# Kernel optimization log

Measured on AMD Instinct MI355X. Metric: run time of the kernel, lower is better.

## Reference

```python
import jax, jax.numpy as jnp
import numpy as np

HEADS = 16
LN_EPS = 1e-6

def _layernorm(x, scale, bias):
    mu = jnp.mean(x, axis=-1, keepdims=True)
    var = jnp.mean(jnp.square(x - mu), axis=-1, keepdims=True)
    return (x - mu) * jax.lax.rsqrt(var + LN_EPS) * scale + bias

def setup_inputs() -> dict:
    key = jax.random.key(0)
    ks = jax.random.split(key, 5)
    B, L, D, F = 2, 2048, 1024, 4096
    s = lambda fan_in: 1.0 / np.sqrt(fan_in)
    return {
        'x': jax.random.normal(ks[0], (B, L, D), jnp.float32),
        'ln1_scale': jnp.ones((D,), jnp.float32),
        'ln1_bias': jnp.zeros((D,), jnp.float32),
        'w_qkv': jax.random.normal(ks[1], (D, 3 * D), jnp.float32) * s(D),
        'w_proj': jax.random.normal(ks[2], (D, D), jnp.float32) * s(D),
        'b_proj': jnp.zeros((D,), jnp.float32),
        'ln2_scale': jnp.ones((D,), jnp.float32),
        'ln2_bias': jnp.zeros((D,), jnp.float32),
        'w_mlp1': jax.random.normal(ks[3], (D, F), jnp.float32) * s(D),
        'b_mlp1': jnp.zeros((F,), jnp.float32),
        'w_mlp2': jax.random.normal(ks[4], (F, D), jnp.float32) * s(F),
        'b_mlp2': jnp.zeros((D,), jnp.float32),
    }

def reference(x, ln1_scale, ln1_bias, w_qkv, w_proj, b_proj,
              ln2_scale, ln2_bias, w_mlp1, b_mlp1, w_mlp2, b_mlp2):
    B, L, D = x.shape
    H = HEADS
    hd = D // H
    # pre-norm attention
    h = _layernorm(x, ln1_scale, ln1_bias)
    qkv = h @ w_qkv  # [B,L,3D]
    q, k, v = jnp.split(qkv, 3, axis=-1)
    q = q.reshape(B, L, H, hd).transpose(0, 2, 1, 3)  # [B,H,L,hd]
    k = k.reshape(B, L, H, hd).transpose(0, 2, 1, 3)
    v = v.reshape(B, L, H, hd).transpose(0, 2, 1, 3)
    scale = jnp.sqrt(jnp.float32(hd))
    scores = jnp.einsum('bhqd,bhkd->bhqk', q, k) / scale  # [B,H,L,L]
    attn = jax.nn.softmax(scores, axis=-1)
    out = jnp.einsum('bhqk,bhkd->bhqd', attn, v)  # [B,H,L,hd]
    out = out.transpose(0, 2, 1, 3).reshape(B, L, D)
    x = x + out @ w_proj + b_proj
    # pre-norm MLP
    h = _layernorm(x, ln2_scale, ln2_bias)
    m = jax.nn.gelu(h @ w_mlp1 + b_mlp1, approximate=True)
    return x + m @ w_mlp2 + b_mlp2
```

## Files before the change

### kernel.cpp

```cpp
#include <hip/hip_runtime.h>
#include <hip/hip_bf16.h>
#include <cstdint>
#include <cstddef>

typedef __bf16 bf16;
typedef __bf16 bf16x8 __attribute__((ext_vector_type(8)));
typedef float f32x4 __attribute__((ext_vector_type(4)));
typedef short short4v __attribute__((ext_vector_type(4)));
typedef unsigned uint2v __attribute__((ext_vector_type(2)));
typedef unsigned uint4v __attribute__((ext_vector_type(4)));

#define GLB_AS(p) ((const __attribute__((address_space(1))) unsigned*)(unsigned long long)(p))
#define LDS_AS(p) ((__attribute__((address_space(3))) unsigned*)(unsigned)(unsigned long long)(p))

__device__ __forceinline__ void g2l16(const void* g, void* l) {
  __builtin_amdgcn_global_load_lds(GLB_AS(g), LDS_AS(l), 16, 0, 0);
}

__device__ __forceinline__ short f2bf(float x) {
  bf16 h = (bf16)x;
  return __builtin_bit_cast(short, h);
}

__device__ __forceinline__ unsigned pk_bf16(float a, float b) {
  __hip_bfloat162 h = __float22bfloat162_rn(float2{a, b});
  unsigned u;
  __builtin_memcpy(&u, &h, 4);
  return u;
}

extern "C" __device__ __attribute__((const)) float __ocml_native_exp2_f32(float);
extern "C" __device__ __attribute__((const)) float __ocml_native_recip_f32(float);
__device__ __forceinline__ float fast_exp2(float x) {
  return __ocml_native_exp2_f32(x);
}
__device__ __forceinline__ float fast_tanh(float a) {
  float e = __ocml_native_exp2_f32(a * 2.8853900817779268f);
  return 1.f - 2.f * __ocml_native_recip_f32(e + 1.f);
}

constexpr int MROWS = 4096;
constexpr size_t ATILE = (size_t)MROWS * 32;

#define QSCALE 0.18033688011112042f

__device__ __forceinline__ void transpose_body(
    const float* __restrict__ in, bf16* __restrict__ out, int K, int N,
    int bx, int by, float (*tile)[33], int tid)
{
  int tx = tid & 31, ty = tid >> 5;
  int n0 = bx * 32, k0 = by * 32;
  for (int i = ty; i < 32; i += 8)
    tile[i][tx] = in[(size_t)(k0 + i) * N + n0 + tx];
  __syncthreads();
  bf16* obase = out + (size_t)(k0 >> 5) * N * 32;
  for (int i = ty; i < 32; i += 8)
    obase[(size_t)(n0 + i) * 32 + tx] = (bf16)tile[tx][i];
}

__device__ __forceinline__ void ln_body(
    const float* __restrict__ x, const float* __restrict__ sc,
    const float* __restrict__ bi, bf16* __restrict__ out,
    int row, float* wsum, float* wsq, int tid)
{
  const float* xr = x + (size_t)row * 1024;
  int c = tid * 4;
  float4 xv = *(const float4*)(xr + c);
  float s = xv.x + xv.y + xv.z + xv.w;
  float q = xv.x * xv.x + xv.y * xv.y + xv.z * xv.z + xv.w * xv.w;
#pragma unroll
  for (int off = 1; off < 64; off <<= 1) {
    s += __shfl_xor(s, off);
    q += __shfl_xor(q, off);
  }
  int wv = tid >> 6;
  if ((tid & 63) == 0) { wsum[wv] = s; wsq[wv] = q; }
  __syncthreads();
  s = wsum[0] + wsum[1] + wsum[2] + wsum[3];
  q = wsq[0] + wsq[1] + wsq[2] + wsq[3];
  float mean = s * (1.f / 1024.f);
  float var = q * (1.f / 1024.f) - mean * mean;
  float rstd = rsqrtf(var + 1e-6f);
  float4 scv = *(const float4*)(sc + c);
  float4 biv = *(const float4*)(bi + c);
  bf16* o = out + (size_t)(c >> 5) * ATILE + (size_t)row * 32 + (c & 31);
  o[0] = (bf16)((xv.x - mean) * rstd * scv.x + biv.x);
  o[1] = (bf16)((xv.y - mean) * rstd * scv.y + biv.y);
  o[2] = (bf16)((xv.z - mean) * rstd * scv.z + biv.z);
  o[3] = (bf16)((xv.w - mean) * rstd * scv.w + biv.w);
}

__global__ __launch_bounds__(256) void prep_kernel(
    const float* __restrict__ wqkv, const float* __restrict__ wproj,
    const float* __restrict__ wmlp1, const float* __restrict__ wmlp2,
    bf16* __restrict__ wqkv_t, bf16* __restrict__ wproj_t,
    bf16* __restrict__ wmlp1_t, bf16* __restrict__ wmlp2_t,
    const float* __restrict__ x, const float* __restrict__ ln1s,
    const float* __restrict__ ln1b, bf16* __restrict__ hbuf)
{
  __shared__ float tile[32][33];
  __shared__ float wsum[4], wsq[4];
  int bid = blockIdx.x, tid = threadIdx.x;
  if (bid < 3072)
    transpose_body(wqkv, wqkv_t, 1024, 3072, bid % 96, bid / 96, tile, tid);
  else if (bid < 4096) {
    int i = bid - 3072;
    transpose_body(wproj, wproj_t, 1024, 1024, i % 32, i / 32, tile, tid);
  } else if (bid < 8192) {
    int i = bid - 4096;
    transpose_body(wmlp1, wmlp1_t, 1024, 4096, i % 128, i / 128, tile, tid);
  } else if (bid < 12288) {
    int i = bid - 8192;
    transpose_body(wmlp2, wmlp2_t, 4096, 1024, i % 32, i / 32, tile, tid);
  } else {
    ln_body(x, ln1s, ln1b, hbuf, bid - 12288, wsum, wsq, tid);
  }
}

__global__ __launch_bounds__(256) void ln_kernel(
    const float* __restrict__ x, const float* __restrict__ sc,
    const float* __restrict__ bi, bf16* __restrict__ out)
{
  __shared__ float wsum[4], wsq[4];
  ln_body(x, sc, bi, out, blockIdx.x, wsum, wsq, threadIdx.x);
}

template <int MT, int NT, int KS, int EPI>
__global__ __launch_bounds__(256) void gemm_tt(
    const bf16* __restrict__ A, const bf16* __restrict__ Bt,
    int N, int K,
    const float* __restrict__ bias, const float* __restrict__ resid,
    float* __restrict__ outf, bf16* __restrict__ ob0,
    bf16* __restrict__ ob1, bf16* __restrict__ ob2)
{
  constexpr int TM = MT * 32, TN = NT * 32;
  __shared__ __align__(16) bf16 As[2][TM * 32 * KS];
  __shared__ __align__(16) bf16 Bs[2][TN * 32 * KS];
  const int tid = threadIdx.x, lane = tid & 63, wave = tid >> 6;
  const int wm = wave >> 1, wn = wave & 1;
  const int quad = lane >> 4, l16 = lane & 15;

  int flat = blockIdx.x + gridDim.x * blockIdx.y;
  int xcd = flat & 7, rr = flat >> 3;
  int npx = gridDim.x >> 3;
  int bn = xcd * npx + (rr % npx);
  int bm = rr / npx;

  const size_t astride = ATILE;
  const size_t bstride = (size_t)N * 32;
  const bf16* Abase = A + (size_t)bm * TM * 32 + (size_t)lane * 8;
  const bf16* Bbase = Bt + (size_t)bn * TN * 32 + (size_t)lane * 8;

  f32x4 acc[MT][NT] = {};
  const int KT = K / (32 * KS);

  auto stage = [&](int buf, int kt) {
#pragma unroll
    for (int ks = 0; ks < KS; ks++) {
      const bf16* Ab = Abase + (size_t)(kt * KS + ks) * astride;
      const bf16* Bb = Bbase + (size_t)(kt * KS + ks) * bstride;
#pragma unroll
      for (int i = 0; i < MT / 2; i++)
        g2l16(Ab + (wave + 4 * i) * 512, &As[buf][ks * TM * 32 + (wave + 4 * i) * 512]);
#pragma unroll
      for (int i = 0; i < NT / 2; i++)
        g2l16(Bb + (wave + 4 * i) * 512, &Bs[buf][ks * TN * 32 + (wave + 4 * i) * 512]);
    }
  };

  stage(0, 0);
  int buf = 0;
  for (int kt = 0; kt < KT; kt++) {
    __syncthreads();
    if (kt + 1 < KT) stage(buf ^ 1, kt + 1);
#pragma unroll
    for (int kk = 0; kk < KS; kk++) {
      bf16x8 af[MT], bfr[NT];
#pragma unroll
      for (int mt = 0; mt < MT; mt++)
        af[mt] = *(const bf16x8*)&As[buf][kk * TM * 32 + (wm * MT * 16 + mt * 16 + l16) * 32 + quad * 8];
#pragma unroll
      for (int nt = 0; nt < NT; nt++)
        bfr[nt] = *(const bf16x8*)&Bs[buf][kk * TN * 32 + (wn * NT * 16 + nt * 16 + l16) * 32 + quad * 8];
#pragma unroll
      for (int mt = 0; mt < MT; mt++)
#pragma unroll
        for (int nt = 0; nt < NT; nt++)
          acc[mt][nt] = __builtin_amdgcn_mfma_f32_16x16x32_bf16(af[mt], bfr[nt], acc[mt][nt], 0, 0, 0);
    }
    buf ^= 1;
  }

#pragma unroll
  for (int mt = 0; mt < MT; mt++) {
#pragma unroll
    for (int nt = 0; nt < NT; nt++) {
      int row0 = bm * TM + wm * MT * 16 + mt * 16 + quad * 4;
      int col = bn * TN + wn * NT * 16 + nt * 16 + l16;
      if (EPI == 0) {
        int b = row0 >> 11, l = row0 & 2047;
        int which = col >> 10, d = col & 1023;
        int hh = d >> 6, hdi = d & 63;
        size_t bh = (size_t)(b * 16 + hh);
        if (which == 0) {
#pragma unroll
          for (int r = 0; r < 4; r++)
            ob0[(bh * 2048 + l + r) * 64 + hdi] = (bf16)(acc[mt][nt][r] * QSCALE);
        } else if (which == 1) {
#pragma unroll
          for (int r = 0; r < 4; r++)
            ob1[(bh * 2048 + l + r) * 64 + hdi] = (bf16)acc[mt][nt][r];
        } else {
          short4v v4;
#pragma unroll
          for (int r = 0; r < 4; r++) v4[r] = f2bf(acc[mt][nt][r]);
          *(short4v*)&ob2[(bh * 64 + hdi) * 2048 + l] = v4;
        }
      } else {
#pragma unroll
        for (int r = 0; r < 4; r++) {
          int row = row0 + r;
          float v = acc[mt][nt][r];
          if (EPI == 1) {
            size_t idx = (size_t)row * N + col;
            outf[idx] = v + bias[col] + resid[idx];
          } else {
            float t = v + bias[col];
            float a = 0.7978845608028654f * t * (1.f + 0.044715f * t * t);
            float g = 0.5f * t * (1.f + fast_tanh(a));
            ob0[(size_t)(col >> 5) * ATILE + (size_t)row * 32 + (col & 31)] = (bf16)g;
          }
        }
      }
    }
  }
}

__global__ __launch_bounds__(512, 2) void gemm8p_gelu(
    const bf16* __restrict__ A, const bf16* __restrict__ Bt,
    const float* __restrict__ bias, bf16* __restrict__ ob0)
{
  __shared__ __align__(16) bf16 As[4 * 8192];
  __shared__ __align__(16) bf16 Bs[4 * 8192];
  const int tid = threadIdx.x, lane = tid & 63, wave = tid >> 6;
  const int quad = lane >> 4, l16 = lane & 15;
  const int wm = wave >> 2, wn = wave & 3;

  int flat = blockIdx.x + gridDim.x * blockIdx.y;
  int xcd = flat & 7, rr = flat >> 3;
  int bn = xcd * 2 + (rr & 1);
  int bm = rr >> 1;

  auto stA = [&](int buf, int ktile, int half) {
    const bf16* g = A + (size_t)ktile * ATILE +
                    ((size_t)bm * 256 + half * 128) * 32 + (size_t)tid * 8;
    g2l16(g, &As[(buf * 2 + (ktile & 1)) * 8192 + half * 4096 + wave * 512]);
  };
  auto stB = [&](int buf, int ktile, int half) {
    const bf16* g = Bt + (size_t)ktile * ATILE +
                    ((size_t)bn * 256 + half * 128) * 32 + (size_t)tid * 8;
    g2l16(g, &Bs[(buf * 2 + (ktile & 1)) * 8192 + half * 4096 + wave * 512]);
  };

  f32x4 acc[8][4] = {};
  bf16x8 af[4][2], bfr[4][2];

  stA(0, 0, 0); stA(0, 0, 1); stA(0, 1, 0); stA(0, 1, 1);
  stB(0, 0, 0); stB(0, 0, 1); stB(0, 1, 0); stB(0, 1, 1);
  asm volatile("s_waitcnt vmcnt(0)" ::: "memory");
  __builtin_amdgcn_s_barrier();

  for (int kt = 0; kt < 16; kt++) {
    const int buf = kt & 1, nbuf = buf ^ 1;
    const bool more = (kt + 1) < 16;
    const int kA = (kt + 1) * 2;

#pragma unroll
    for (int mt = 0; mt < 4; mt++)
#pragma unroll
      for (int kk = 0; kk < 2; kk++)
        af[mt][kk] = *(const bf16x8*)&As[(buf * 2 + kk) * 8192 +
                       (wm * 128 + mt * 16 + l16) * 32 + quad * 8];
#pragma unroll
    for (int nt = 0; nt < 2; nt++)
#pragma unroll
      for (int kk = 0; kk < 2; kk++)
        bfr[nt][kk] = *(const bf16x8*)&Bs[(buf * 2 + kk) * 8192 +
                        (wn * 64 + nt * 16 + l16) * 32 + quad * 8];
    if (more) { stA(nbuf, kA, 0); stA(nbuf, kA, 1); stA(nbuf, kA + 1, 0); stA(nbuf, kA + 1, 1); }
    __builtin_amdgcn_s_barrier();
    asm volatile("s_waitcnt lgkmcnt(0)" ::: "memory");
    __builtin_amdgcn_sched_barrier(0);
    __builtin_amdgcn_s_setprio(1);
#pragma unroll
    for (int mt = 0; mt < 4; mt++)
#pragma unroll
      for (int nt = 0; nt < 2; nt++)
#pragma unroll
        for (int kk = 0; kk < 2; kk++)
          acc[mt][nt] = __builtin_amdgcn_mfma_f32_16x16x32_bf16(af[mt][kk], bfr[nt][kk], acc[mt][nt], 0, 0, 0);
    __builtin_amdgcn_s_setprio(0);
    __builtin_amdgcn_s_barrier();

#pragma unroll
    for (int nt = 2; nt < 4; nt++)
#pragma unroll
      for (int kk = 0; kk < 2; kk++)
        bfr[nt][kk] = *(const bf16x8*)&Bs[(buf * 2 + kk) * 8192 +
                        (wn * 64 + nt * 16 + l16) * 32 + quad * 8];
    if (more) { stB(nbuf, kA, 0); stB(nbuf, kA, 1); stB(nbuf, kA + 1, 0); stB(nbuf, kA + 1, 1); }
    __builtin_amdgcn_s_barrier();
    asm volatile("s_waitcnt lgkmcnt(0)" ::: "memory");
    __builtin_amdgcn_sched_barrier(0);
    __builtin_amdgcn_s_setprio(1);
#pragma unroll
    for (int mt = 0; mt < 4; mt++)
#pragma unroll
      for (int nt = 2; nt < 4; nt++)
#pragma unroll
        for (int kk = 0; kk < 2; kk++)
          acc[mt][nt] = __builtin_amdgcn_mfma_f32_16x16x32_bf16(af[mt][kk], bfr[nt][kk], acc[mt][nt], 0, 0, 0);
    __builtin_amdgcn_s_setprio(0);
    __builtin_amdgcn_s_barrier();

#pragma unroll
    for (int mt = 0; mt < 4; mt++)
#pragma unroll
      for (int kk = 0; kk < 2; kk++)
        af[mt][kk] = *(const bf16x8*)&As[(buf * 2 + kk) * 8192 +
                       (wm * 128 + (mt + 4) * 16 + l16) * 32 + quad * 8];
    __builtin_amdgcn_s_barrier();
    asm volatile("s_waitcnt lgkmcnt(0)" ::: "memory");
    __builtin_amdgcn_sched_barrier(0);
    __builtin_amdgcn_s_setprio(1);
#pragma unroll
    for (int mt = 0; mt < 4; mt++)
#pragma unroll
      for (int nt = 0; nt < 2; nt++)
#pragma unroll
        for (int kk = 0; kk < 2; kk++)
          acc[mt + 4][nt] = __builtin_amdgcn_mfma_f32_16x16x32_bf16(af[mt][kk], bfr[nt][kk], acc[mt + 4][nt], 0, 0, 0);
    __builtin_amdgcn_s_setprio(0);
    __builtin_amdgcn_s_barrier();

    __builtin_amdgcn_s_setprio(1);
#pragma unroll
    for (int mt = 0; mt < 4; mt++)
#pragma unroll
      for (int nt = 2; nt < 4; nt++)
#pragma unroll
        for (int kk = 0; kk < 2; kk++)
          acc[mt + 4][nt] = __builtin_amdgcn_mfma_f32_16x16x32_bf16(af[mt][kk], bfr[nt][kk], acc[mt + 4][nt], 0, 0, 0);
    __builtin_amdgcn_s_setprio(0);
    asm volatile("s_waitcnt vmcnt(0)" ::: "memory");
    __builtin_amdgcn_s_barrier();
  }

#pragma unroll
  for (int mt = 0; mt < 8; mt++) {
#pragma unroll
    for (int nt = 0; nt < 4; nt++) {
      int row0 = bm * 256 + wm * 128 + mt * 16 + quad * 4;
      int col = bn * 256 + wn * 64 + nt * 16 + l16;
      float bcol = bias[col];
#pragma unroll
      for (int r = 0; r < 4; r++) {
        int row = row0 + r;
        float t = acc[mt][nt][r] + bcol;
        float a = 0.7978845608028654f * t * (1.f + 0.044715f * t * t);
        float g = 0.5f * t * (1.f + fast_tanh(a));
        ob0[(size_t)(col >> 5) * ATILE + (size_t)row * 32 + (col & 31)] = (bf16)g;
      }
    }
  }
}

__global__ __launch_bounds__(256, 2) void flash_attn(
    const bf16* __restrict__ Q, const bf16* __restrict__ Kg,
    const bf16* __restrict__ Vg, bf16* __restrict__ O)
{
  __shared__ __align__(16) bf16 Ks[128 * 64];
  __shared__ __align__(16) bf16 Vs[64 * 128];
  const int tid = threadIdx.x, lane = tid & 63, wave = tid >> 6;
  const int quad = lane >> 4, l16 = lane & 15;
  const int qt = blockIdx.x, bh = blockIdx.y;
  const int b = bh >> 4, h = bh & 15;

  const bf16* qg = Q + ((size_t)bh * 2048 + qt * 128) * 64;
  const bf16* kg = Kg + (size_t)bh * 2048 * 64;
  const bf16* vg = Vg + (size_t)bh * 64 * 2048;

  const int a0 = tid >> 3;
  const int a5 = a0 & 31;
  const int vb = ((a5 >> 2) & 1) * 16 + (a5 >> 3) * 4 + (a5 & 3);
  const int v0 = (a0 & ~31) + vb;
  const int kw0 = (v0 << 7) + (((tid & 7) << 4) ^ ((v0 & 7) << 4));
  const int vw0 = ((tid >> 4) << 8) + (((tid & 15) << 4) ^ (((tid >> 4) & 7) << 4));

  bf16x8 qf[2][2];
#pragma unroll
  for (int s = 0; s < 2; s++)
#pragma unroll
    for (int kk = 0; kk < 2; kk++)
      qf[s][kk] = *(const bf16x8*)&qg[(size_t)(wave * 32 + s * 16 + l16) * 64 + kk * 32 + quad * 8];

  f32x4 oacc[2][4] = {};
  float lrow[2] = {0.f, 0.f};

  bf16x8 kreg[4], vreg[4];
#pragma unroll
  for (int i = 0; i < 4; i++) {
    int t = tid + i * 256;
    kreg[i] = *(const bf16x8*)&kg[(size_t)(t >> 3) * 64 + (t & 7) * 8];
    vreg[i] = *(const bf16x8*)&vg[(size_t)(t >> 4) * 2048 + (t & 15) * 8];
  }

  for (int kt = 0; kt < 16; kt++) {
    __syncthreads();
#pragma unroll
    for (int i = 0; i < 4; i++) {
      *(bf16x8*)((char*)Ks + kw0 + i * 4096) = kreg[i];
      *(bf16x8*)((char*)Vs + vw0 + i * 4096) = vreg[i];
    }
    __syncthreads();
    if (kt < 15) {
#pragma unroll
      for (int i = 0; i < 4; i++) {
        int t = tid + i * 256;
        kreg[i] = *(const bf16x8*)&kg[((size_t)(kt + 1) * 128 + (t >> 3)) * 64 + (t & 7) * 8];
        vreg[i] = *(const bf16x8*)&vg[(size_t)(t >> 4) * 2048 + (kt + 1) * 128 + (t & 15) * 8];
      }
    }

    f32x4 sacc[2][8] = {};
#pragma unroll
    for (int kk = 0; kk < 2; kk++) {
#pragma unroll
      for (int ct = 0; ct < 8; ct++) {
        int krow = ct * 16 + l16;
        bf16x8 kf = *(const bf16x8*)((const char*)Ks + krow * 128 +
                                     ((kk * 64 + quad * 16) ^ ((l16 & 7) << 4)));
        sacc[0][ct] = __builtin_amdgcn_mfma_f32_16x16x32_bf16(kf, qf[0][kk], sacc[0][ct], 0, 0, 0);
        sacc[1][ct] = __builtin_amdgcn_mfma_f32_16x16x32_bf16(kf, qf[1][kk], sacc[1][ct], 0, 0, 0);
      }
    }

    bf16x8 pf[2][4];
#pragma unroll
    for (int s = 0; s < 2; s++) {
      float sum = 0.f;
#pragma unroll
      for (int c = 0; c < 4; c++) {
        uint4v u;
#pragma unroll
        for (int bb = 0; bb < 2; bb++) {
          float p0 = fast_exp2(sacc[s][2 * c + bb][0]);
          float p1 = fast_exp2(sacc[s][2 * c + bb][1]);
          float p2 = fast_exp2(sacc[s][2 * c + bb][2]);
          float p3 = fast_exp2(sacc[s][2 * c + bb][3]);
          sum += (p0 + p1) + (p2 + p3);
          u[bb * 2 + 0] = pk_bf16(p0, p1);
          u[bb * 2 + 1] = pk_bf16(p2, p3);
        }
        pf[s][c] = __builtin_bit_cast(bf16x8, u);
      }
      lrow[s] += sum;
    }

#pragma unroll
    for (int ot = 0; ot < 4; ot++) {
#pragma unroll
      for (int c = 0; c < 4; c++) {
        int vrow = ot * 16 + l16;
        bf16x8 vf = *(const bf16x8*)((const char*)Vs + vrow * 256 +
                                     ((c * 64 + quad * 16) ^ ((l16 & 7) << 4)));
        oacc[0][ot] = __builtin_amdgcn_mfma_f32_16x16x32_bf16(vf, pf[0][c], oacc[0][ot], 0, 0, 0);
        oacc[1][ot] = __builtin_amdgcn_mfma_f32_16x16x32_bf16(vf, pf[1][c], oacc[1][ot], 0, 0, 0);
      }
    }
  }

#pragma unroll
  for (int s = 0; s < 2; s++) {
    float l = lrow[s];
    l += __shfl_xor(l, 16);
    l += __shfl_xor(l, 32);
    float inv = 1.f / l;
    int qrow = qt * 128 + wave * 32 + s * 16 + l16;
    size_t grow = (size_t)b * 2048 + qrow;
#pragma unroll
    for (int ot = 0; ot < 4; ot++) {
      int col = h * 64 + ot * 16 + quad * 4;
      short4v o4;
#pragma unroll
      for (int r = 0; r < 4; r++) o4[r] = f2bf(oacc[s][ot][r] * inv);
      *(short4v*)&O[(size_t)(col >> 5) * ATILE + grow * 32 + (col & 31)] = o4;
    }
  }
}

extern "C" void kernel_launch(void* const* d_in, const int* in_sizes, int n_in,
                              void* d_out, int out_size, void* d_ws, size_t ws_size,
                              hipStream_t stream)
{
  const float* x     = (const float*)d_in[0];
  const float* ln1s  = (const float*)d_in[1];
  const float* ln1b  = (const float*)d_in[2];
  const float* wqkv  = (const float*)d_in[3];
  const float* wproj = (const float*)d_in[4];
  const float* bproj = (const float*)d_in[5];
  const float* ln2s  = (const float*)d_in[6];
  const float* ln2b  = (const float*)d_in[7];
  const float* wmlp1 = (const float*)d_in[8];
  const float* bmlp1 = (const float*)d_in[9];
  const float* wmlp2 = (const float*)d_in[10];
  const float* bmlp2 = (const float*)d_in[11];
  float* out = (float*)d_out;

  char* ws = (char*)d_ws;
  bf16* wqkv_t  = (bf16*)(ws + 0);
  bf16* wproj_t = (bf16*)(ws + 6291456);
  bf16* wmlp1_t = (bf16*)(ws + 8388608);
  bf16* wmlp2_t = (bf16*)(ws + 16777216);
  bf16* hbuf    = (bf16*)(ws + 25165824);
  bf16* qb      = (bf16*)(ws + 33554432);
  bf16* kb      = (bf16*)(ws + 41943040);
  bf16* vb      = (bf16*)(ws + 50331648);
  bf16* aout    = (bf16*)(ws + 58720256);
  bf16* mbuf    = (bf16*)(ws + 33554432);

  prep_kernel<<<16384, 256, 0, stream>>>(wqkv, wproj, wmlp1, wmlp2,
                                         wqkv_t, wproj_t, wmlp1_t, wmlp2_t,
                                         x, ln1s, ln1b, hbuf);
  gemm_tt<4, 4, 1, 0><<<dim3(24, 32), 256, 0, stream>>>(hbuf, wqkv_t, 3072, 1024,
                                                        nullptr, nullptr, nullptr, qb, kb, vb);
  flash_attn<<<dim3(16, 32), 256, 0, stream>>>(qb, kb, vb, aout);
  gemm_tt<2, 4, 2, 1><<<dim3(8, 64), 256, 0, stream>>>(aout, wproj_t, 1024, 1024,
                                                       bproj, x, out, nullptr, nullptr, nullptr);
  ln_kernel<<<4096, 256, 0, stream>>>(out, ln2s, ln2b, hbuf);
  gemm8p_gelu<<<dim3(16, 16), 512, 0, stream>>>(hbuf, wmlp1_t, bmlp1, mbuf);
  gemm_tt<2, 4, 2, 1><<<dim3(8, 64), 256, 0, stream>>>(mbuf, wmlp2_t, 1024, 4096,
                                                       bmlp2, out, out, nullptr, nullptr, nullptr);
}
```

Measured before the change: 310.3 us.

## Use 256x256 eight-wave pipelined GEMM for the QKV projection

```diff
diff --git a/kernel.cpp b/kernel.cpp
--- a/kernel.cpp
+++ b/kernel.cpp
@@ -197,40 +197,12 @@
     for (int nt = 0; nt < NT; nt++) {
       int row0 = bm * TM + wm * MT * 16 + mt * 16 + quad * 4;
       int col = bn * TN + wn * NT * 16 + nt * 16 + l16;
-      if (EPI == 0) {
-        int b = row0 >> 11, l = row0 & 2047;
-        int which = col >> 10, d = col & 1023;
-        int hh = d >> 6, hdi = d & 63;
-        size_t bh = (size_t)(b * 16 + hh);
-        if (which == 0) {
-#pragma unroll
-          for (int r = 0; r < 4; r++)
-            ob0[(bh * 2048 + l + r) * 64 + hdi] = (bf16)(acc[mt][nt][r] * QSCALE);
-        } else if (which == 1) {
-#pragma unroll
-          for (int r = 0; r < 4; r++)
-            ob1[(bh * 2048 + l + r) * 64 + hdi] = (bf16)acc[mt][nt][r];
-        } else {
-          short4v v4;
-#pragma unroll
-          for (int r = 0; r < 4; r++) v4[r] = f2bf(acc[mt][nt][r]);
-          *(short4v*)&ob2[(bh * 64 + hdi) * 2048 + l] = v4;
-        }
-      } else {
-#pragma unroll
-        for (int r = 0; r < 4; r++) {
-          int row = row0 + r;
-          float v = acc[mt][nt][r];
-          if (EPI == 1) {
-            size_t idx = (size_t)row * N + col;
-            outf[idx] = v + bias[col] + resid[idx];
-          } else {
-            float t = v + bias[col];
-            float a = 0.7978845608028654f * t * (1.f + 0.044715f * t * t);
-            float g = 0.5f * t * (1.f + fast_tanh(a));
-            ob0[(size_t)(col >> 5) * ATILE + (size_t)row * 32 + (col & 31)] = (bf16)g;
-          }
-        }
+#pragma unroll
+      for (int r = 0; r < 4; r++) {
+        int row = row0 + r;
+        float v = acc[mt][nt][r];
+        size_t idx = (size_t)row * N + col;
+        outf[idx] = v + bias[col] + resid[idx];
       }
     }
   }
@@ -370,6 +342,156 @@
         float a = 0.7978845608028654f * t * (1.f + 0.044715f * t * t);
         float g = 0.5f * t * (1.f + fast_tanh(a));
         ob0[(size_t)(col >> 5) * ATILE + (size_t)row * 32 + (col & 31)] = (bf16)g;
+      }
+    }
+  }
+}
+
+__global__ __launch_bounds__(512, 2) void gemm8p_qkv(
+    const bf16* __restrict__ A, const bf16* __restrict__ Bt,
+    bf16* __restrict__ ob0, bf16* __restrict__ ob1, bf16* __restrict__ ob2)
+{
+  __shared__ __align__(16) bf16 As[4 * 8192];
+  __shared__ __align__(16) bf16 Bs[4 * 8192];
+  const int tid = threadIdx.x, lane = tid & 63, wave = tid >> 6;
+  const int quad = lane >> 4, l16 = lane & 15;
+  const int wm = wave >> 2, wn = wave & 3;
+
+  int flat = blockIdx.x + gridDim.x * blockIdx.y;
+  int xcd = flat & 7, rr = flat >> 3;
+  int wg = xcd * 24 + rr;
+  int bm = wg & 15, bn = wg >> 4;
+
+  const size_t BSTR = (size_t)3072 * 32;
+
+  auto stA = [&](int buf, int ktile, int half) {
+    const bf16* g = A + (size_t)ktile * ATILE +
+                    ((size_t)bm * 256 + half * 128) * 32 + (size_t)tid * 8;
+    g2l16(g, &As[(buf * 2 + (ktile & 1)) * 8192 + half * 4096 + wave * 512]);
+  };
+  auto stB = [&](int buf, int ktile, int half) {
+    const bf16* g = Bt + (size_t)ktile * BSTR +
+                    ((size_t)bn * 256 + half * 128) * 32 + (size_t)tid * 8;
+    g2l16(g, &Bs[(buf * 2 + (ktile & 1)) * 8192 + half * 4096 + wave * 512]);
+  };
+
+  f32x4 acc[8][4] = {};
+  bf16x8 af[4][2], bfr[4][2];
+
+  stA(0, 0, 0); stA(0, 0, 1); stA(0, 1, 0); stA(0, 1, 1);
+  stB(0, 0, 0); stB(0, 0, 1); stB(0, 1, 0); stB(0, 1, 1);
+  asm volatile("s_waitcnt vmcnt(0)" ::: "memory");
+  __builtin_amdgcn_s_barrier();
+
+  for (int kt = 0; kt < 16; kt++) {
+    const int buf = kt & 1, nbuf = buf ^ 1;
+    const bool more = (kt + 1) < 16;
+    const int kA = (kt + 1) * 2;
+
+#pragma unroll
+    for (int mt = 0; mt < 4; mt++)
+#pragma unroll
+      for (int kk = 0; kk < 2; kk++)
+        af[mt][kk] = *(const bf16x8*)&As[(buf * 2 + kk) * 8192 +
+                       (wm * 128 + mt * 16 + l16) * 32 + quad * 8];
+#pragma unroll
+    for (int nt = 0; nt < 2; nt++)
+#pragma unroll
+      for (int kk = 0; kk < 2; kk++)
+        bfr[nt][kk] = *(const bf16x8*)&Bs[(buf * 2 + kk) * 8192 +
+                        (wn * 64 + nt * 16 + l16) * 32 + quad * 8];
+    if (more) { stA(nbuf, kA, 0); stA(nbuf, kA, 1); stA(nbuf, kA + 1, 0); stA(nbuf, kA + 1, 1); }
+    __builtin_amdgcn_s_barrier();
+    asm volatile("s_waitcnt lgkmcnt(0)" ::: "memory");
+    __builtin_amdgcn_sched_barrier(0);
+    __builtin_amdgcn_s_setprio(1);
+#pragma unroll
+    for (int mt = 0; mt < 4; mt++)
+#pragma unroll
+      for (int nt = 0; nt < 2; nt++)
+#pragma unroll
+        for (int kk = 0; kk < 2; kk++)
+          acc[mt][nt] = __builtin_amdgcn_mfma_f32_16x16x32_bf16(af[mt][kk], bfr[nt][kk], acc[mt][nt], 0, 0, 0);
+    __builtin_amdgcn_s_setprio(0);
+    __builtin_amdgcn_s_barrier();
+
+#pragma unroll
+    for (int nt = 2; nt < 4; nt++)
+#pragma unroll
+      for (int kk = 0; kk < 2; kk++)
+        bfr[nt][kk] = *(const bf16x8*)&Bs[(buf * 2 + kk) * 8192 +
+                        (wn * 64 + nt * 16 + l16) * 32 + quad * 8];
+    if (more) { stB(nbuf, kA, 0); stB(nbuf, kA, 1); stB(nbuf, kA + 1, 0); stB(nbuf, kA + 1, 1); }
+    __builtin_amdgcn_s_barrier();
+    asm volatile("s_waitcnt lgkmcnt(0)" ::: "memory");
+    __builtin_amdgcn_sched_barrier(0);
+    __builtin_amdgcn_s_setprio(1);
+#pragma unroll
+    for (int mt = 0; mt < 4; mt++)
+#pragma unroll
+      for (int nt = 2; nt < 4; nt++)
+#pragma unroll
+        for (int kk = 0; kk < 2; kk++)
+          acc[mt][nt] = __builtin_amdgcn_mfma_f32_16x16x32_bf16(af[mt][kk], bfr[nt][kk], acc[mt][nt], 0, 0, 0);
+    __builtin_amdgcn_s_setprio(0);
+    __builtin_amdgcn_s_barrier();
+
+#pragma unroll
+    for (int mt = 0; mt < 4; mt++)
+#pragma unroll
+      for (int kk = 0; kk < 2; kk++)
+        af[mt][kk] = *(const bf16x8*)&As[(buf * 2 + kk) * 8192 +
+                       (wm * 128 + (mt + 4) * 16 + l16) * 32 + quad * 8];
+    __builtin_amdgcn_s_barrier();
+    asm volatile("s_waitcnt lgkmcnt(0)" ::: "memory");
+    __builtin_amdgcn_sched_barrier(0);
+    __builtin_amdgcn_s_setprio(1);
+#pragma unroll
+    for (int mt = 0; mt < 4; mt++)
+#pragma unroll
+      for (int nt = 0; nt < 2; nt++)
+#pragma unroll
+        for (int kk = 0; kk < 2; kk++)
+          acc[mt + 4][nt] = __builtin_amdgcn_mfma_f32_16x16x32_bf16(af[mt][kk], bfr[nt][kk], acc[mt + 4][nt], 0, 0, 0);
+    __builtin_amdgcn_s_setprio(0);
+    __builtin_amdgcn_s_barrier();
+
+    __builtin_amdgcn_s_setprio(1);
+#pragma unroll
+    for (int mt = 0; mt < 4; mt++)
+#pragma unroll
+      for (int nt = 2; nt < 4; nt++)
+#pragma unroll
+        for (int kk = 0; kk < 2; kk++)
+          acc[mt + 4][nt] = __builtin_amdgcn_mfma_f32_16x16x32_bf16(af[mt][kk], bfr[nt][kk], acc[mt + 4][nt], 0, 0, 0);
+    __builtin_amdgcn_s_setprio(0);
+    asm volatile("s_waitcnt vmcnt(0)" ::: "memory");
+    __builtin_amdgcn_s_barrier();
+  }
+
+#pragma unroll
+  for (int mt = 0; mt < 8; mt++) {
+#pragma unroll
+    for (int nt = 0; nt < 4; nt++) {
+      int row0 = bm * 256 + wm * 128 + mt * 16 + quad * 4;
+      int col = bn * 256 + wn * 64 + nt * 16 + l16;
+      int b = row0 >> 11, l = row0 & 2047;
+      int which = col >> 10, d = col & 1023;
+      int hh = d >> 6, hdi = d & 63;
+      size_t bh = (size_t)(b * 16 + hh);
+      if (which == 0) {
+#pragma unroll
+        for (int r = 0; r < 4; r++)
+          ob0[(bh * 2048 + l + r) * 64 + hdi] = (bf16)(acc[mt][nt][r] * QSCALE);
+      } else if (which == 1) {
+#pragma unroll
+        for (int r = 0; r < 4; r++)
+          ob1[(bh * 2048 + l + r) * 64 + hdi] = (bf16)acc[mt][nt][r];
+      } else {
+        short4v v4;
+#pragma unroll
+        for (int r = 0; r < 4; r++) v4[r] = f2bf(acc[mt][nt][r]);
+        *(short4v*)&ob2[(bh * 64 + hdi) * 2048 + l] = v4;
       }
     }
   }
@@ -532,8 +654,7 @@
   prep_kernel<<<16384, 256, 0, stream>>>(wqkv, wproj, wmlp1, wmlp2,
                                          wqkv_t, wproj_t, wmlp1_t, wmlp2_t,
                                          x, ln1s, ln1b, hbuf);
-  gemm_tt<4, 4, 1, 0><<<dim3(24, 32), 256, 0, stream>>>(hbuf, wqkv_t, 3072, 1024,
-                                                        nullptr, nullptr, nullptr, qb, kb, vb);
+  gemm8p_qkv<<<dim3(12, 16), 512, 0, stream>>>(hbuf, wqkv_t, qb, kb, vb);
   flash_attn<<<dim3(16, 32), 256, 0, stream>>>(qb, kb, vb, aout);
   gemm_tt<2, 4, 2, 1><<<dim3(8, 64), 256, 0, stream>>>(aout, wproj_t, 1024, 1024,
                                                        bproj, x, out, nullptr, nullptr, nullptr);
```

Measured after the change: 316.5 us. 1.02x slower.

## Software-pipeline flash attention PV matmul one tile behind QK^T with double-buffered V

Applied to the files above, without the earlier changes.

```diff
diff --git a/kernel.cpp b/kernel.cpp
--- a/kernel.cpp
+++ b/kernel.cpp
@@ -221,15 +221,8 @@
         for (int r = 0; r < 4; r++) {
           int row = row0 + r;
           float v = acc[mt][nt][r];
-          if (EPI == 1) {
-            size_t idx = (size_t)row * N + col;
-            outf[idx] = v + bias[col] + resid[idx];
-          } else {
-            float t = v + bias[col];
-            float a = 0.7978845608028654f * t * (1.f + 0.044715f * t * t);
-            float g = 0.5f * t * (1.f + fast_tanh(a));
-            ob0[(size_t)(col >> 5) * ATILE + (size_t)row * 32 + (col & 31)] = (bf16)g;
-          }
+          size_t idx = (size_t)row * N + col;
+          outf[idx] = v + bias[col] + resid[idx];
         }
       }
     }
@@ -380,7 +373,7 @@
     const bf16* __restrict__ Vg, bf16* __restrict__ O)
 {
   __shared__ __align__(16) bf16 Ks[128 * 64];
-  __shared__ __align__(16) bf16 Vs[64 * 128];
+  __shared__ __align__(16) bf16 Vs[2][64 * 128];
   const int tid = threadIdx.x, lane = tid & 63, wave = tid >> 6;
   const int quad = lane >> 4, l16 = lane & 15;
   const int qt = blockIdx.x, bh = blockIdx.y;
@@ -406,6 +399,7 @@
 
   f32x4 oacc[2][4] = {};
   float lrow[2] = {0.f, 0.f};
+  bf16x8 pf0[2][4], pf1[2][4];
 
   bf16x8 kreg[4], vreg[4];
 #pragma unroll
@@ -415,15 +409,16 @@
     vreg[i] = *(const bf16x8*)&vg[(size_t)(t >> 4) * 2048 + (t & 15) * 8];
   }
 
-  for (int kt = 0; kt < 16; kt++) {
+  auto step = [&](int kt, int vbuf, bf16x8 (&pfP)[2][4],
+                  bf16x8 (&pfC)[2][4], bool doPV) {
     __syncthreads();
 #pragma unroll
     for (int i = 0; i < 4; i++) {
       *(bf16x8*)((char*)Ks + kw0 + i * 4096) = kreg[i];
-      *(bf16x8*)((char*)Vs + vw0 + i * 4096) = vreg[i];
+      *(bf16x8*)((char*)&Vs[vbuf][0] + vw0 + i * 4096) = vreg[i];
     }
     __syncthreads();
-    if (kt < 15) {
+    if (kt + 1 < 16) {
 #pragma unroll
       for (int i = 0; i < 4; i++) {
         int t = tid + i * 256;
@@ -445,7 +440,20 @@
       }
     }
 
-    bf16x8 pf[2][4];
+    if (doPV) {
+#pragma unroll
+      for (int ot = 0; ot < 4; ot++) {
+#pragma unroll
+        for (int c = 0; c < 4; c++) {
+          int vrow = ot * 16 + l16;
+          bf16x8 vf = *(const bf16x8*)((const char*)&Vs[vbuf ^ 1][0] + vrow * 256 +
+                                       ((c * 64 + quad * 16) ^ ((l16 & 7) << 4)));
+          oacc[0][ot] = __builtin_amdgcn_mfma_f32_16x16x32_bf16(vf, pfP[0][c], oacc[0][ot], 0, 0, 0);
+          oacc[1][ot] = __builtin_amdgcn_mfma_f32_16x16x32_bf16(vf, pfP[1][c], oacc[1][ot], 0, 0, 0);
+        }
+      }
+    }
+
 #pragma unroll
     for (int s = 0; s < 2; s++) {
       float sum = 0.f;
@@ -462,21 +470,26 @@
           u[bb * 2 + 0] = pk_bf16(p0, p1);
           u[bb * 2 + 1] = pk_bf16(p2, p3);
         }
-        pf[s][c] = __builtin_bit_cast(bf16x8, u);
+        pfC[s][c] = __builtin_bit_cast(bf16x8, u);
       }
       lrow[s] += sum;
     }
-
-#pragma unroll
-    for (int ot = 0; ot < 4; ot++) {
-#pragma unroll
-      for (int c = 0; c < 4; c++) {
-        int vrow = ot * 16 + l16;
-        bf16x8 vf = *(const bf16x8*)((const char*)Vs + vrow * 256 +
-                                     ((c * 64 + quad * 16) ^ ((l16 & 7) << 4)));
-        oacc[0][ot] = __builtin_amdgcn_mfma_f32_16x16x32_bf16(vf, pf[0][c], oacc[0][ot], 0, 0, 0);
-        oacc[1][ot] = __builtin_amdgcn_mfma_f32_16x16x32_bf16(vf, pf[1][c], oacc[1][ot], 0, 0, 0);
-      }
+  };
+
+  for (int k2 = 0; k2 < 8; k2++) {
+    step(2 * k2,     0, pf1, pf0, k2 > 0);
+    step(2 * k2 + 1, 1, pf0, pf1, true);
+  }
+
+#pragma unroll
+  for (int ot = 0; ot < 4; ot++) {
+#pragma unroll
+    for (int c = 0; c < 4; c++) {
+      int vrow = ot * 16 + l16;
+      bf16x8 vf = *(const bf16x8*)((const char*)&Vs[1][0] + vrow * 256 +
+                                   ((c * 64 + quad * 16) ^ ((l16 & 7) << 4)));
+      oacc[0][ot] = __builtin_amdgcn_mfma_f32_16x16x32_bf16(vf, pf1[0][c], oacc[0][ot], 0, 0, 0);
+      oacc[1][ot] = __builtin_amdgcn_mfma_f32_16x16x32_bf16(vf, pf1[1][c], oacc[1][ot], 0, 0, 0);
     }
   }
 
```

After: 308.7 us. Within noise of the previous version (-0.5%).
